# Kernel optimization log

Hardware: AMD Instinct MI355X
Metric: run time of the kernel (lower is better)

The kernel has to match this reference:

```python
import jax, jax.numpy as jnp
import numpy as np

VOCAB = 131072
EMB_DIM = 2048
N_PAD = 2048  # next power of two >= EMB_DIM
CB = 65536    # 2^16 codebook entries of E8 (8-dim) vectors


def fht(x):
    """Unnormalized fast Hadamard transform over the last dim (power of 2)."""
    n = x.shape[-1]
    orig = x.shape
    x = x.reshape(-1, n)
    h = 1
    while h < n:
        x = x.reshape(-1, n // (2 * h), 2, h)
        a, b = x[:, :, 0, :], x[:, :, 1, :]
        x = jnp.stack([a + b, a - b], axis=2).reshape(-1, n)
        h *= 2
    return x.reshape(orig)


def setup_inputs() -> dict:
    key = jax.random.key(0)
    k = jax.random.split(key, 6)
    input_ids = jax.random.randint(k[0], (8, 2048), 0, VOCAB, dtype=jnp.int32)
    Qidxs = jax.random.randint(k[1], (VOCAB, N_PAD // 8), -32768, 32768, dtype=jnp.int32).astype(jnp.int16)
    Qidxs2 = jax.random.randint(k[2], (VOCAB, N_PAD // 8), -32768, 32768, dtype=jnp.int32).astype(jnp.int16)
    codebook = (jax.random.normal(k[3], (CB, 8), dtype=jnp.float32) * 0.5).astype(jnp.float16)
    codebook2 = (jax.random.normal(k[4], (CB, 8), dtype=jnp.float32) * 0.5).astype(jnp.float16)
    SV = (jax.random.uniform(k[5], (N_PAD,), dtype=jnp.float32) * 0.5 + 0.75).astype(jnp.float16)
    Wscale = jnp.asarray(0.02, dtype=jnp.float32)
    inv_resid_scale = jnp.asarray(0.3, dtype=jnp.float32)
    return {"input_ids": input_ids, "Qidxs": Qidxs, "Qidxs2": Qidxs2,
            "codebook": codebook, "codebook2": codebook2, "SV": SV,
            "Wscale": Wscale, "inv_resid_scale": inv_resid_scale}


def reference(input_ids, Qidxs, Qidxs2, codebook, codebook2, SV, Wscale, inv_resid_scale):
    flat = input_ids.reshape(-1)                 # [N]
    n_tok = flat.shape[0]
    # stage 1: row gather -> packed int16 -> codebook gather
    rows1 = Qidxs[flat]                          # [N, N_PAD//8] int16
    idx1 = (rows1.astype(jnp.int32) & 0xFFFF).reshape(-1)
    deq = codebook[idx1].reshape(n_tok, N_PAD).astype(jnp.float32)
    # stage 2 residual
    rows2 = Qidxs2[flat]
    idx2 = (rows2.astype(jnp.int32) & 0xFFFF).reshape(-1)
    deq2 = codebook2[idx2].reshape(n_tok, N_PAD).astype(jnp.float32)
    deq = deq + deq2 * inv_resid_scale
    deq = deq * Wscale
    deq = fht(deq)
    deq = deq * SV.astype(jnp.float32)
    out = deq[:, :EMB_DIM].astype(jnp.float16)   # out dtype = SV.dtype
    return out.reshape(input_ids.shape + (EMB_DIM,))
```

## Files before the change

kernel.cpp:

```cpp
#include <hip/hip_runtime.h>

constexpr int WPB = 4;

__global__ __launch_bounds__(256, 4) void e8rht_kernel(
    const int* __restrict__ input_ids,
    const int* __restrict__ Qidxs,
    const int* __restrict__ Qidxs2,
    const float* __restrict__ codebook,
    const float* __restrict__ codebook2,
    const float* __restrict__ SV,
    const float* __restrict__ Wscale,
    const float* __restrict__ inv_resid,
    float* __restrict__ out)
{
    __shared__ __align__(16) float lds[WPB * 2048];
    const int wave = threadIdx.x >> 6;
    const int lane = threadIdx.x & 63;
    const int tok  = blockIdx.x * WPB + wave;

    const float ws  = Wscale[0];
    const float ws2 = ws * inv_resid[0];
    const int tid = input_ids[tok];

    const int4 q1 = *(const int4*)(Qidxs  + tid * 256 + lane * 4);
    const int4 q2 = *(const int4*)(Qidxs2 + tid * 256 + lane * 4);

    float v[32];
    {
        const int i1[4] = { q1.x & 0xFFFF, q1.y & 0xFFFF, q1.z & 0xFFFF, q1.w & 0xFFFF };
        const int i2[4] = { q2.x & 0xFFFF, q2.y & 0xFFFF, q2.z & 0xFFFF, q2.w & 0xFFFF };
        #pragma unroll
        for (int c = 0; c < 4; ++c) {
            const float4* r1 = (const float4*)(codebook  + (size_t)i1[c] * 8);
            const float4* r2 = (const float4*)(codebook2 + (size_t)i2[c] * 8);
            const float4 a0 = r1[0], a1 = r1[1];
            const float4 b0 = r2[0], b1 = r2[1];
            v[8*c + 0] = a0.x * ws + b0.x * ws2;
            v[8*c + 1] = a0.y * ws + b0.y * ws2;
            v[8*c + 2] = a0.z * ws + b0.z * ws2;
            v[8*c + 3] = a0.w * ws + b0.w * ws2;
            v[8*c + 4] = a1.x * ws + b1.x * ws2;
            v[8*c + 5] = a1.y * ws + b1.y * ws2;
            v[8*c + 6] = a1.z * ws + b1.z * ws2;
            v[8*c + 7] = a1.w * ws + b1.w * ws2;
        }
    }

    #pragma unroll
    for (int h = 1; h < 32; h <<= 1) {
        #pragma unroll
        for (int r = 0; r < 32; ++r) {
            if ((r & h) == 0) {
                float a = v[r], b = v[r + h];
                v[r] = a + b;
                v[r + h] = a - b;
            }
        }
    }

    float* L = lds + wave * 2048;
    {
        const int t4 = lane >> 2, tl = lane & 3;
        #pragma unroll
        for (int j = 0; j < 32; ++j) {
            const int col = (((t4 ^ (j & 15)) << 2) | tl);
            L[(j << 6) + col] = v[j];
        }
    }
    __syncthreads();

    const int j0 = lane >> 1;
    const int b  = lane & 1;
    float w[32];
    {
        const float4* Lr = (const float4*)(L + (j0 << 6));
        #pragma unroll
        for (int c = 0; c < 8; ++c) {
            const int ch = ((b << 3) + c) ^ (j0 & 15);
            const float4 f = Lr[ch];
            w[4*c + 0] = f.x; w[4*c + 1] = f.y; w[4*c + 2] = f.z; w[4*c + 3] = f.w;
        }
    }

    #pragma unroll
    for (int h = 1; h < 32; h <<= 1) {
        #pragma unroll
        for (int r = 0; r < 32; ++r) {
            if ((r & h) == 0) {
                float a = w[r], bb = w[r + h];
                w[r] = a + bb;
                w[r + h] = a - bb;
            }
        }
    }

    #pragma unroll
    for (int r = 0; r < 32; ++r) {
        const float o = __shfl_xor(w[r], 1, 64);
        w[r] = b ? (o - w[r]) : (w[r] + o);
    }

    const size_t obase = (size_t)tok * 2048;
    const int ebase = (b << 10) | j0;
    #pragma unroll
    for (int r = 0; r < 32; ++r) {
        const int e = ebase + (r << 5);
        out[obase + e] = w[r] * SV[e];
    }
}

extern "C" void kernel_launch(void* const* d_in, const int* in_sizes, int n_in,
                              void* d_out, int out_size, void* d_ws, size_t ws_size,
                              hipStream_t stream) {
    const int* input_ids   = (const int*)d_in[0];
    const int* Qidxs       = (const int*)d_in[1];
    const int* Qidxs2      = (const int*)d_in[2];
    const float* codebook  = (const float*)d_in[3];
    const float* codebook2 = (const float*)d_in[4];
    const float* SV        = (const float*)d_in[5];
    const float* wscale    = (const float*)d_in[6];
    const float* irs       = (const float*)d_in[7];
    float* out             = (float*)d_out;

    const int n_tok = in_sizes[0];
    const int grid  = n_tok / WPB;
    e8rht_kernel<<<grid, 256, 0, stream>>>(input_ids, Qidxs, Qidxs2,
                                           codebook, codebook2, SV,
                                           wscale, irs, out);
}
```

Before: 341.9 us.

## Convert codebooks to fp16 in workspace and gather half-width entries

Adds a pre-pass kernel that converts both fp32 codebooks into packed fp16 copies in the workspace, so each gathered 8-element entry is 16 bytes instead of 32. The main kernel then unpacks the halves to float. It also uses nontemporal loads for the Qidxs rows and nontemporal stores for the output. The block barrier is replaced with a wave barrier, since each wave only touches its own LDS slice. This costs an extra kernel launch and a conversion pass on every call, and falls back to the fp32 path when the workspace is too small.

Result: faster. 319.5 us (-6.5%).

```diff
diff --git a/kernel.cpp b/kernel.cpp
--- a/kernel.cpp
+++ b/kernel.cpp
@@ -1,8 +1,139 @@
 #include <hip/hip_runtime.h>
+#include <hip/hip_fp16.h>
 
 constexpr int WPB = 4;
 
-__global__ __launch_bounds__(256, 4) void e8rht_kernel(
+typedef int   v4i __attribute__((ext_vector_type(4)));
+typedef unsigned int v4u __attribute__((ext_vector_type(4)));
+
+__global__ __launch_bounds__(256) void cvt_kernel(
+    const float* __restrict__ cb1, const float* __restrict__ cb2,
+    unsigned int* __restrict__ o1, unsigned int* __restrict__ o2)
+{
+    const int r = blockIdx.x * 256 + threadIdx.x;
+    const float* src = (r < 65536) ? (cb1 + (size_t)r * 8)
+                                   : (cb2 + (size_t)(r - 65536) * 8);
+    unsigned int* dst = (r < 65536) ? (o1 + (size_t)r * 4)
+                                    : (o2 + (size_t)(r - 65536) * 4);
+    const float4 a = ((const float4*)src)[0];
+    const float4 b = ((const float4*)src)[1];
+    __half2 h0 = __floats2half2_rn(a.x, a.y);
+    __half2 h1 = __floats2half2_rn(a.z, a.w);
+    __half2 h2 = __floats2half2_rn(b.x, b.y);
+    __half2 h3 = __floats2half2_rn(b.z, b.w);
+    v4u o;
+    o.x = *(unsigned int*)&h0; o.y = *(unsigned int*)&h1;
+    o.z = *(unsigned int*)&h2; o.w = *(unsigned int*)&h3;
+    *(v4u*)dst = o;
+}
+
+__global__ __launch_bounds__(256, 4) void e8rht_kernel_h(
+    const int* __restrict__ input_ids,
+    const int* __restrict__ Qidxs,
+    const int* __restrict__ Qidxs2,
+    const unsigned int* __restrict__ cb1h,
+    const unsigned int* __restrict__ cb2h,
+    const float* __restrict__ SV,
+    const float* __restrict__ Wscale,
+    const float* __restrict__ inv_resid,
+    float* __restrict__ out)
+{
+    __shared__ __align__(16) float lds[WPB * 2048];
+    const int wave = threadIdx.x >> 6;
+    const int lane = threadIdx.x & 63;
+    const int tok  = blockIdx.x * WPB + wave;
+
+    const float ws  = Wscale[0];
+    const float ws2 = ws * inv_resid[0];
+    const int tid = input_ids[tok];
+
+    const v4i q1 = __builtin_nontemporal_load((const v4i*)(Qidxs  + (size_t)tid * 256 + lane * 4));
+    const v4i q2 = __builtin_nontemporal_load((const v4i*)(Qidxs2 + (size_t)tid * 256 + lane * 4));
+
+    float v[32];
+    {
+        const int i1[4] = { q1.x & 0xFFFF, q1.y & 0xFFFF, q1.z & 0xFFFF, q1.w & 0xFFFF };
+        const int i2[4] = { q2.x & 0xFFFF, q2.y & 0xFFFF, q2.z & 0xFFFF, q2.w & 0xFFFF };
+        #pragma unroll
+        for (int c = 0; c < 4; ++c) {
+            const v4u a = *(const v4u*)(cb1h + (size_t)i1[c] * 4);
+            const v4u b = *(const v4u*)(cb2h + (size_t)i2[c] * 4);
+            const unsigned int au[4] = { a.x, a.y, a.z, a.w };
+            const unsigned int bu[4] = { b.x, b.y, b.z, b.w };
+            #pragma unroll
+            for (int p = 0; p < 4; ++p) {
+                const float2 fa = __half22float2(*(const __half2*)&au[p]);
+                const float2 fb = __half22float2(*(const __half2*)&bu[p]);
+                v[8*c + 2*p]     = fa.x * ws + fb.x * ws2;
+                v[8*c + 2*p + 1] = fa.y * ws + fb.y * ws2;
+            }
+        }
+    }
+
+    #pragma unroll
+    for (int h = 1; h < 32; h <<= 1) {
+        #pragma unroll
+        for (int r = 0; r < 32; ++r) {
+            if ((r & h) == 0) {
+                float a = v[r], b = v[r + h];
+                v[r] = a + b;
+                v[r + h] = a - b;
+            }
+        }
+    }
+
+    float* L = lds + wave * 2048;
+    {
+        const int t4 = lane >> 2, tl = lane & 3;
+        #pragma unroll
+        for (int j = 0; j < 32; ++j) {
+            const int col = (((t4 ^ (j & 15)) << 2) | tl);
+            L[(j << 6) + col] = v[j];
+        }
+    }
+    __builtin_amdgcn_wave_barrier();
+
+    const int j0 = lane >> 1;
+    const int b  = lane & 1;
+    float w[32];
+    {
+        const float4* Lr = (const float4*)(L + (j0 << 6));
+        #pragma unroll
+        for (int c = 0; c < 8; ++c) {
+            const int ch = ((b << 3) + c) ^ (j0 & 15);
+            const float4 f = Lr[ch];
+            w[4*c + 0] = f.x; w[4*c + 1] = f.y; w[4*c + 2] = f.z; w[4*c + 3] = f.w;
+        }
+    }
+
+    #pragma unroll
+    for (int h = 1; h < 32; h <<= 1) {
+        #pragma unroll
+        for (int r = 0; r < 32; ++r) {
+            if ((r & h) == 0) {
+                float a = w[r], bb = w[r + h];
+                w[r] = a + bb;
+                w[r + h] = a - bb;
+            }
+        }
+    }
+
+    #pragma unroll
+    for (int r = 0; r < 32; ++r) {
+        const float o = __shfl_xor(w[r], 1, 64);
+        w[r] = b ? (o - w[r]) : (w[r] + o);
+    }
+
+    const size_t obase = (size_t)tok * 2048;
+    const int ebase = (b << 10) | j0;
+    #pragma unroll
+    for (int r = 0; r < 32; ++r) {
+        const int e = ebase + (r << 5);
+        __builtin_nontemporal_store(w[r] * SV[e], &out[obase + e]);
+    }
+}
+
+__global__ __launch_bounds__(256, 4) void e8rht_kernel_f(
     const int* __restrict__ input_ids,
     const int* __restrict__ Qidxs,
     const int* __restrict__ Qidxs2,
@@ -22,8 +153,8 @@
     const float ws2 = ws * inv_resid[0];
     const int tid = input_ids[tok];
 
-    const int4 q1 = *(const int4*)(Qidxs  + tid * 256 + lane * 4);
-    const int4 q2 = *(const int4*)(Qidxs2 + tid * 256 + lane * 4);
+    const int4 q1 = *(const int4*)(Qidxs  + (size_t)tid * 256 + lane * 4);
+    const int4 q2 = *(const int4*)(Qidxs2 + (size_t)tid * 256 + lane * 4);
 
     float v[32];
     {
@@ -35,40 +166,26 @@
             const float4* r2 = (const float4*)(codebook2 + (size_t)i2[c] * 8);
             const float4 a0 = r1[0], a1 = r1[1];
             const float4 b0 = r2[0], b1 = r2[1];
-            v[8*c + 0] = a0.x * ws + b0.x * ws2;
-            v[8*c + 1] = a0.y * ws + b0.y * ws2;
-            v[8*c + 2] = a0.z * ws + b0.z * ws2;
-            v[8*c + 3] = a0.w * ws + b0.w * ws2;
-            v[8*c + 4] = a1.x * ws + b1.x * ws2;
-            v[8*c + 5] = a1.y * ws + b1.y * ws2;
-            v[8*c + 6] = a1.z * ws + b1.z * ws2;
-            v[8*c + 7] = a1.w * ws + b1.w * ws2;
-        }
-    }
-
-    #pragma unroll
-    for (int h = 1; h < 32; h <<= 1) {
-        #pragma unroll
-        for (int r = 0; r < 32; ++r) {
-            if ((r & h) == 0) {
-                float a = v[r], b = v[r + h];
-                v[r] = a + b;
-                v[r + h] = a - b;
-            }
-        }
-    }
+            v[8*c+0]=a0.x*ws+b0.x*ws2; v[8*c+1]=a0.y*ws+b0.y*ws2;
+            v[8*c+2]=a0.z*ws+b0.z*ws2; v[8*c+3]=a0.w*ws+b0.w*ws2;
+            v[8*c+4]=a1.x*ws+b1.x*ws2; v[8*c+5]=a1.y*ws+b1.y*ws2;
+            v[8*c+6]=a1.z*ws+b1.z*ws2; v[8*c+7]=a1.w*ws+b1.w*ws2;
+        }
+    }
+    #pragma unroll
+    for (int h = 1; h < 32; h <<= 1)
+        #pragma unroll
+        for (int r = 0; r < 32; ++r)
+            if ((r & h) == 0) { float a=v[r],b=v[r+h]; v[r]=a+b; v[r+h]=a-b; }
 
     float* L = lds + wave * 2048;
     {
         const int t4 = lane >> 2, tl = lane & 3;
         #pragma unroll
-        for (int j = 0; j < 32; ++j) {
-            const int col = (((t4 ^ (j & 15)) << 2) | tl);
-            L[(j << 6) + col] = v[j];
-        }
+        for (int j = 0; j < 32; ++j)
+            L[(j << 6) + (((t4 ^ (j & 15)) << 2) | tl)] = v[j];
     }
     __syncthreads();
-
     const int j0 = lane >> 1;
     const int b  = lane & 1;
     float w[32];
@@ -76,30 +193,20 @@
         const float4* Lr = (const float4*)(L + (j0 << 6));
         #pragma unroll
         for (int c = 0; c < 8; ++c) {
-            const int ch = ((b << 3) + c) ^ (j0 & 15);
-            const float4 f = Lr[ch];
-            w[4*c + 0] = f.x; w[4*c + 1] = f.y; w[4*c + 2] = f.z; w[4*c + 3] = f.w;
-        }
-    }
-
-    #pragma unroll
-    for (int h = 1; h < 32; h <<= 1) {
-        #pragma unroll
-        for (int r = 0; r < 32; ++r) {
-            if ((r & h) == 0) {
-                float a = w[r], bb = w[r + h];
-                w[r] = a + bb;
-                w[r + h] = a - bb;
-            }
-        }
-    }
-
+            const float4 f = Lr[((b << 3) + c) ^ (j0 & 15)];
+            w[4*c+0]=f.x; w[4*c+1]=f.y; w[4*c+2]=f.z; w[4*c+3]=f.w;
+        }
+    }
+    #pragma unroll
+    for (int h = 1; h < 32; h <<= 1)
+        #pragma unroll
+        for (int r = 0; r < 32; ++r)
+            if ((r & h) == 0) { float a=w[r],bb=w[r+h]; w[r]=a+bb; w[r+h]=a-bb; }
     #pragma unroll
     for (int r = 0; r < 32; ++r) {
         const float o = __shfl_xor(w[r], 1, 64);
         w[r] = b ? (o - w[r]) : (w[r] + o);
     }
-
     const size_t obase = (size_t)tok * 2048;
     const int ebase = (b << 10) | j0;
     #pragma unroll
@@ -124,7 +231,17 @@
 
     const int n_tok = in_sizes[0];
     const int grid  = n_tok / WPB;
-    e8rht_kernel<<<grid, 256, 0, stream>>>(input_ids, Qidxs, Qidxs2,
-                                           codebook, codebook2, SV,
-                                           wscale, irs, out);
-}
+
+    const size_t cb_h_bytes = (size_t)65536 * 8 * 2;
+    if (ws_size >= 2 * cb_h_bytes) {
+        unsigned int* cb1h = (unsigned int*)d_ws;
+        unsigned int* cb2h = (unsigned int*)((char*)d_ws + cb_h_bytes);
+        cvt_kernel<<<512, 256, 0, stream>>>(codebook, codebook2, cb1h, cb2h);
+        e8rht_kernel_h<<<grid, 256, 0, stream>>>(input_ids, Qidxs, Qidxs2,
+                                                 cb1h, cb2h, SV, wscale, irs, out);
+    } else {
+        e8rht_kernel_f<<<grid, 256, 0, stream>>>(input_ids, Qidxs, Qidxs2,
+                                                 codebook, codebook2, SV,
+                                                 wscale, irs, out);
+    }
+}
```
